# Kernel tuning notes

Hardware: AMD Instinct MI355X
Metric: run time of the kernel (lower is better)

## Reference

```python
import jax, jax.numpy as jnp
import numpy as np

N_ATOMS = 8_000_000
N_REC = 2_000_000
N_POC = 500_000
N_CHAINS = 4


def setup_inputs() -> dict:
    key = jax.random.key(0)
    k1, k2, k3, k4 = jax.random.split(key, 4)
    # coordinates in nm, inside a ~5 nm box
    positions = jax.random.uniform(k1, (N_ATOMS, 3), dtype=jnp.float32) * 5.0
    box_vectors = jnp.diag(jnp.array([5.0, 5.0, 5.0], dtype=jnp.float32))
    # unique receptor atom indices into positions
    rec_indices = jax.random.permutation(k2, N_ATOMS)[:N_REC].astype(jnp.int32)
    # unique pocket indices INTO THE REC ARRAY (poc_pos = rec_pos[poc_indices])
    poc_indices = jax.random.permutation(k3, N_REC)[:N_POC].astype(jnp.int32)
    # contiguous chain assignment over rec atoms, all chains present in pocket
    chain_ids = ((jnp.arange(N_REC, dtype=jnp.int32) * N_CHAINS) // N_REC).astype(jnp.int32)
    poc_chain_ids = chain_ids[poc_indices]
    ref_poc = jax.random.uniform(k4, (N_POC, 3), dtype=jnp.float32) * 5.0
    k = jnp.float32(100.0)  # kJ/mol/nm^2
    return {
        "positions": positions, "box_vectors": box_vectors, "ref_poc": ref_poc,
        "k": k, "rec_indices": rec_indices, "poc_indices": poc_indices,
        "chain_ids": chain_ids, "poc_chain_ids": poc_chain_ids, "n_chains": N_CHAINS,
    }


def best_periodic_translation(pos1, pos2, box_vectors):
    # pos1, pos2: [C,3]; box_vectors: [3,3] (rows are lattice vectors)
    delta = pos2 - pos1
    inv = 1.0 / jnp.diag(box_vectors)
    s3 = jnp.round(delta[:, 2] * inv[2])
    delta = delta - s3[:, None] * box_vectors[2]
    s2 = jnp.round(delta[:, 1] * inv[1])
    delta = delta - s2[:, None] * box_vectors[1]
    s1 = jnp.round(delta[:, 0] * inv[0])
    return s1[:, None] * box_vectors[0] + s2[:, None] * box_vectors[1] + s3[:, None] * box_vectors[2]


def reference(positions, box_vectors, ref_poc, k, rec_indices, poc_indices, chain_ids, poc_chain_ids, n_chains):
    rec_pos = positions[rec_indices]  # [R,3]
    # Per-chain pocket COM. NOTE: original indexes global positions here
    # (positions[poc_chain_indices]), NOT rec_pos -- reproduced faithfully.
    poc_glob = positions[poc_indices]  # [P,3]
    counts = jax.ops.segment_sum(jnp.ones((poc_glob.shape[0],), poc_glob.dtype), poc_chain_ids, num_segments=n_chains)  # [C]
    poc_com = jax.ops.segment_sum(poc_glob, poc_chain_ids, num_segments=n_chains) / counts[:, None]  # [C,3]
    ref_com = jax.ops.segment_sum(ref_poc, poc_chain_ids, num_segments=n_chains) / counts[:, None]  # [C,3]
    best_t = best_periodic_translation(poc_com, ref_com, box_vectors)  # [C,3]
    rec_pos = rec_pos + best_t[chain_ids]  # translate each chain into the reference image

    poc_pos = rec_pos[poc_indices]  # [P,3]
    rec_origin = jnp.mean(rec_pos, axis=0)
    rec_centered = rec_pos - rec_origin
    r_sq = jnp.sum(rec_centered ** 2, axis=1)  # [R]
    F = jnp.zeros_like(rec_pos).at[poc_indices].set(-2.0 * k * (poc_pos - ref_poc))
    F_mean = jnp.mean(F, axis=0)
    torque = jnp.cross(rec_centered, F)
    torque_mean = jnp.mean(torque, axis=0)
    F_rot = jnp.cross(torque_mean[None], rec_centered) / r_sq[:, None]
    F_final = jnp.zeros_like(positions).at[rec_indices].set(F_mean + F_rot)
    return (jnp.float32(0.0), F_final)
```

## Files before the change

kernel.cpp:

```cpp
#include <hip/hip_runtime.h>


typedef unsigned int uint32;
typedef unsigned char uchar;

#define MAXC 16
#define W_BT 0
#define W_O 48
#define W_FM 52
#define W_TM 56
#define W_ACC 64

#define GCOUNT_OFF 4096
#define REC_OFF 8192
#define NB 512
#define BSH 14
#define BUCKET_ATOMS (1 << BSH)
#define CAP 5120
#define INV8_OFF (REC_OFF + NB * CAP * 4)

#define PB 512
#define RB 512
#define K1_KPT 16
#define K1_CHUNK (256 * K1_KPT)

struct PartSh { uint32 hist[NB]; uint32 curs[NB]; uint32 base[NB]; };
struct PocSh  { float red[4][43]; float accL[3 + MAXC * 10]; };
union ShU { PartSh part; PocSh poc; };

__device__ inline float waveSum(float v) {
#pragma unroll
  for (int off = 32; off > 0; off >>= 1) v += __shfl_down(v, off, 64);
  return v;
}

__global__ __launch_bounds__(256) void k_fused(
    const float* __restrict__ pos, const float* __restrict__ ref_poc,
    const int* __restrict__ rec_idx, const int* __restrict__ cid,
    const int* __restrict__ poc_idx, const int* __restrict__ poc_cid,
    const int* __restrict__ ncp, int R, int P,
    uint32* __restrict__ gcount, uint32* __restrict__ grecords,
    float* __restrict__ ws) {
  const int tid = threadIdx.x;
  const int bid = blockIdx.x;
  __shared__ ShU sh;
  const int C = ncp[0];

  if (bid < PB) {
    const int gsz = PB * 256;
    if (C <= 4) {
      float vals[43];
#pragma unroll
      for (int v = 0; v < 43; ++v) vals[v] = 0.f;
      for (int rb = bid * 256 + tid; rb < P; rb += 4 * gsz) {
        int rr[4], i2[4], c2[4], ri[4];
        float g[4][3], p[4][3], rf[4][3];
#pragma unroll
        for (int q = 0; q < 4; ++q) {
          int r = rb + q * gsz;
          rr[q] = (r < P) ? r : -1;
        }
#pragma unroll
        for (int q = 0; q < 4; ++q) {
          int r = (rr[q] < 0) ? 0 : rr[q];
          i2[q] = poc_idx[r];
          c2[q] = poc_cid[r];
        }
#pragma unroll
        for (int q = 0; q < 4; ++q) {
          ri[q] = rec_idx[i2[q]];
          g[q][0] = pos[3 * i2[q] + 0];
          g[q][1] = pos[3 * i2[q] + 1];
          g[q][2] = pos[3 * i2[q] + 2];
        }
#pragma unroll
        for (int q = 0; q < 4; ++q) {
          int r = (rr[q] < 0) ? 0 : rr[q];
          p[q][0] = pos[3 * ri[q] + 0];
          p[q][1] = pos[3 * ri[q] + 1];
          p[q][2] = pos[3 * ri[q] + 2];
          rf[q][0] = ref_poc[3 * r + 0];
          rf[q][1] = ref_poc[3 * r + 1];
          rf[q][2] = ref_poc[3 * r + 2];
        }
#pragma unroll
        for (int q = 0; q < 4; ++q) {
          if (rr[q] >= 0) {
            vals[0] += p[q][1] * rf[q][2] - p[q][2] * rf[q][1];
            vals[1] += p[q][2] * rf[q][0] - p[q][0] * rf[q][2];
            vals[2] += p[q][0] * rf[q][1] - p[q][1] * rf[q][0];
#pragma unroll
            for (int cc = 0; cc < 4; ++cc) {
              bool m = (c2[q] == cc);
              float* a = &vals[3 + cc * 10];
              a[0] += m ? g[q][0] : 0.f; a[1] += m ? g[q][1] : 0.f;
              a[2] += m ? g[q][2] : 0.f;
              a[3] += m ? rf[q][0] : 0.f; a[4] += m ? rf[q][1] : 0.f;
              a[5] += m ? rf[q][2] : 0.f;
              a[6] += m ? p[q][0] : 0.f; a[7] += m ? p[q][1] : 0.f;
              a[8] += m ? p[q][2] : 0.f;
              a[9] += m ? 1.f : 0.f;
            }
          }
        }
      }
      const int wid = tid >> 6;
#pragma unroll
      for (int v = 0; v < 43; ++v) {
        float s = waveSum(vals[v]);
        if ((tid & 63) == 0) sh.poc.red[wid][v] = s;
      }
      __syncthreads();
      for (int t = tid; t < 43; t += 256)
        atomicAdd(&ws[W_ACC + 19 + t], sh.poc.red[0][t] + sh.poc.red[1][t] +
                                       sh.poc.red[2][t] + sh.poc.red[3][t]);
    } else {
      float* accL = sh.poc.accL;
      for (int t = tid; t < 3 + MAXC * 10; t += 256) accL[t] = 0.f;
      __syncthreads();
      for (int r = bid * 256 + tid; r < P; r += PB * 256) {
        int i2 = poc_idx[r];
        int c2 = poc_cid[r];
        int ri = rec_idx[i2];
        float gx = pos[3 * i2 + 0], gy = pos[3 * i2 + 1], gz = pos[3 * i2 + 2];
        float px = pos[3 * ri + 0], py = pos[3 * ri + 1], pz = pos[3 * ri + 2];
        float rx = ref_poc[3 * r + 0], ry = ref_poc[3 * r + 1], rz = ref_poc[3 * r + 2];
        atomicAdd(&accL[0], py * rz - pz * ry);
        atomicAdd(&accL[1], pz * rx - px * rz);
        atomicAdd(&accL[2], px * ry - py * rx);
        float* a = &accL[3 + c2 * 10];
        atomicAdd(&a[0], gx); atomicAdd(&a[1], gy); atomicAdd(&a[2], gz);
        atomicAdd(&a[3], rx); atomicAdd(&a[4], ry); atomicAdd(&a[5], rz);
        atomicAdd(&a[6], px); atomicAdd(&a[7], py); atomicAdd(&a[8], pz);
        atomicAdd(&a[9], 1.f);
      }
      __syncthreads();
      for (int t = tid; t < 3 + MAXC * 10; t += 256)
        if (accL[t] != 0.f) atomicAdd(&ws[W_ACC + 19 + t], accL[t]);
    }
  } else {
    const int pb = bid - PB;
    uint32* hist = sh.part.hist;
    uint32* curs = sh.part.curs;
    uint32* base = sh.part.base;
    for (int r0 = pb * K1_CHUNK; r0 < R; r0 += RB * K1_CHUNK) {
      int cnt = R - r0; if (cnt > K1_CHUNK) cnt = K1_CHUNK;
      for (int t = tid; t < NB; t += 256) { hist[t] = 0u; curs[t] = 0u; }
      __syncthreads();
      uint32 enc[K1_KPT];
#pragma unroll
      for (int j = 0; j < K1_KPT; ++j) {
        int t = tid + j * 256;
        uint32 e = 0xFFFFFFFFu;
        if (t < cnt) {
          uint32 idx = (uint32)rec_idx[r0 + t];
          uint32 c = (uint32)cid[r0 + t] & 255u;
          e = (idx << 8) | c;
          atomicAdd(&hist[idx >> BSH], 1u);
        }
        enc[j] = e;
      }
      __syncthreads();
      for (int t = tid; t < NB; t += 256) {
        uint32 h = hist[t];
        base[t] = h ? atomicAdd(&gcount[t], h) : 0u;
      }
      __syncthreads();
#pragma unroll
      for (int j = 0; j < K1_KPT; ++j) {
        uint32 e = enc[j];
        if (e != 0xFFFFFFFFu) {
          uint32 b = e >> (8 + BSH);
          uint32 slot = base[b] + atomicAdd(&curs[b], 1u);
          if (slot < CAP) grecords[b * CAP + slot] = e;
        }
      }
      __syncthreads();
    }
  }
}

__global__ __launch_bounds__(256) void k_bucket_build(
    const float4* __restrict__ pos4, const int* __restrict__ ncp,
    const uint32* __restrict__ gcount, const uint32* __restrict__ grecords,
    int N, uchar* __restrict__ inv8, float* __restrict__ ws) {
  const int tid = threadIdx.x;
  const int b = blockIdx.x;
  const int a0 = b << BSH;
  if (a0 >= N) return;
  int natoms = N - a0; if (natoms > BUCKET_ATOMS) natoms = BUCKET_ATOMS;

  __shared__ uchar map_[BUCKET_ATOMS];
  __shared__ float cnt16[MAXC];
  uint4* m16 = (uint4*)map_;
  uint4 ff; ff.x = ff.y = ff.z = ff.w = 0xFFFFFFFFu;
  for (int t = tid; t < BUCKET_ATOMS / 16; t += 256) m16[t] = ff;
  const int C = ncp[0];
  if (C > 4) for (int t = tid; t < MAXC; t += 256) cnt16[t] = 0.f;
  __syncthreads();

  int n = (int)gcount[b]; if (n > CAP) n = CAP;
  float c0 = 0.f, c1 = 0.f, c2 = 0.f, c3 = 0.f;
  for (int t = tid; t < n; t += 256) {
    uint32 e = grecords[b * CAP + t];
    uint32 ia = (e >> 8) & (BUCKET_ATOMS - 1);
    uint32 c = e & 255u;
    map_[ia] = (uchar)c;
    if (C <= 4) {
      c0 += (c == 0u) ? 1.f : 0.f;
      c1 += (c == 1u) ? 1.f : 0.f;
      c2 += (c == 2u) ? 1.f : 0.f;
      c3 += (c == 3u) ? 1.f : 0.f;
    } else {
      atomicAdd(&cnt16[c], 1.f);
    }
  }
  __syncthreads();

  uchar* dst = inv8 + a0;
  if (natoms == BUCKET_ATOMS) {
    uint4* d16 = (uint4*)dst;
    for (int t = tid; t < BUCKET_ATOMS / 16; t += 256) d16[t] = m16[t];
  } else {
    for (int t = tid; t < natoms; t += 256) dst[t] = map_[t];
  }

  float sx = 0.f, sy = 0.f, sz = 0.f;
  int ngf = natoms >> 2;
  const uchar4* m4 = (const uchar4*)map_;
  int g0 = a0 >> 2;
  for (int g = tid; g < ngf; g += 256) {
    float4 p0 = pos4[3 * (g0 + g) + 0];
    float4 p1 = pos4[3 * (g0 + g) + 1];
    float4 p2 = pos4[3 * (g0 + g) + 2];
    uchar4 m = m4[g];
    if (m.x != 255) { sx += p0.x; sy += p0.y; sz += p0.z; }
    if (m.y != 255) { sx += p0.w; sy += p1.x; sz += p1.y; }
    if (m.z != 255) { sx += p1.z; sy += p1.w; sz += p2.x; }
    if (m.w != 255) { sx += p2.y; sy += p2.z; sz += p2.w; }
  }
  int tb = natoms & 3;
  if (tid < tb) {
    int a = a0 + (ngf << 2) + tid;
    const float* pf = (const float*)pos4;
    if (map_[(ngf << 2) + tid] != 255) {
      sx += pf[3 * a]; sy += pf[3 * a + 1]; sz += pf[3 * a + 2];
    }
  }

  __shared__ float red[4][7];
  float vv[7] = {sx, sy, sz, c0, c1, c2, c3};
  const int wid = tid >> 6;
#pragma unroll
  for (int v = 0; v < 7; ++v) {
    float s = waveSum(vv[v]);
    if ((tid & 63) == 0) red[wid][v] = s;
  }
  __syncthreads();
  if (tid < 7) {
    float s = red[0][tid] + red[1][tid] + red[2][tid] + red[3][tid];
    atomicAdd(&ws[W_ACC + tid], s);
  }
  if (C > 4 && tid < C) atomicAdd(&ws[W_ACC + 3 + tid], cnt16[tid]);
}

__global__ void k_finalize(const float* __restrict__ box,
                           const float* __restrict__ kp,
                           const int* __restrict__ ncp,
                           int R, float* __restrict__ ws) {
  __shared__ float tot[192];
  const int C = ncp[0];
  for (int t = threadIdx.x; t < 192; t += blockDim.x) tot[t] = ws[W_ACC + t];
  __syncthreads();
  if (threadIdx.x != 0) return;
  const float kk = kp[0];
  const float Rf = (float)R;
  const float* xp = &tot[19];
  float inv0 = 1.f / box[0], inv1 = 1.f / box[4], inv2 = 1.f / box[8];
  float ox = tot[0], oy = tot[1], oz = tot[2];
  float Fx = 0, Fy = 0, Fz = 0;
  float T1x = 0, T1y = 0, T1z = 0, T2x = 0, T2y = 0, T2z = 0;
  for (int c = 0; c < C; ++c) {
    float nrec = tot[3 + c];
    const float* a = &tot[22 + c * 10];
    float np = a[9];
    float invn = 1.f / np;
    float pcx = a[0] * invn, pcy = a[1] * invn, pcz = a[2] * invn;
    float rcx = a[3] * invn, rcy = a[4] * invn, rcz = a[5] * invn;
    float dx = rcx - pcx, dy = rcy - pcy, dz = rcz - pcz;
    float s3 = rintf(dz * inv2);
    dx -= s3 * box[6]; dy -= s3 * box[7]; dz -= s3 * box[8];
    float s2 = rintf(dy * inv1);
    dx -= s2 * box[3]; dy -= s2 * box[4]; dz -= s2 * box[5];
    float s1 = rintf(dx * inv0);
    float btx = s1 * box[0] + s2 * box[3] + s3 * box[6];
    float bty = s1 * box[1] + s2 * box[4] + s3 * box[7];
    float btz = s1 * box[2] + s2 * box[5] + s3 * box[8];
    ws[W_BT + c * 3 + 0] = btx;
    ws[W_BT + c * 3 + 1] = bty;
    ws[W_BT + c * 3 + 2] = btz;
    ox += nrec * btx; oy += nrec * bty; oz += nrec * btz;
    float SFx = -2.f * kk * (a[6] + np * btx - a[3]);
    float SFy = -2.f * kk * (a[7] + np * bty - a[4]);
    float SFz = -2.f * kk * (a[8] + np * btz - a[5]);
    Fx += SFx; Fy += SFy; Fz += SFz;
    T1x += a[7] * btz - a[8] * bty;
    T1y += a[8] * btx - a[6] * btz;
    T1z += a[6] * bty - a[7] * btx;
    T2x += bty * SFz - btz * SFy;
    T2y += btz * SFx - btx * SFz;
    T2z += btx * SFy - bty * SFx;
  }
  ox /= Rf; oy /= Rf; oz /= Rf;
  float Tx = 2.f * kk * xp[0] - 2.f * kk * T1x + T2x - (oy * Fz - oz * Fy);
  float Ty = 2.f * kk * xp[1] - 2.f * kk * T1y + T2y - (oz * Fx - ox * Fz);
  float Tz = 2.f * kk * xp[2] - 2.f * kk * T1z + T2z - (ox * Fy - oy * Fx);
  ws[W_O + 0] = ox; ws[W_O + 1] = oy; ws[W_O + 2] = oz;
  ws[W_FM + 0] = Fx / Rf; ws[W_FM + 1] = Fy / Rf; ws[W_FM + 2] = Fz / Rf;
  ws[W_TM + 0] = Tx / Rf; ws[W_TM + 1] = Ty / Rf; ws[W_TM + 2] = Tz / Rf;
}

__global__ __launch_bounds__(256) void k_final_dense(
    const float* __restrict__ pos, const uchar* __restrict__ inv8,
    int N, const float* __restrict__ ws, float* __restrict__ out) {
  __shared__ float stage[3328];
  __shared__ float sc[64];
  const int tid = threadIdx.x;
  if (tid < 64) sc[tid] = ws[tid];
  const int t0 = blockIdx.x * 1024;
  int nat = N - t0; if (nat > 1024) nat = 1024;
  const int nfl = nat * 3;

  if (nat == 1024) {
    const float4* src4 = (const float4*)(pos + 3 * t0);
#pragma unroll
    for (int kk = 0; kk < 3; ++kk) {
      int v4 = tid + kk * 256;
      float4 p = src4[v4];
      int idx = 4 * v4 + v4 / 3;
      stage[idx + 0] = p.x; stage[idx + 1] = p.y;
      stage[idx + 2] = p.z; stage[idx + 3] = p.w;
    }
  } else {
    for (int k = tid; k < nfl; k += 256)
      stage[k + (int)((unsigned)k / 12u)] = pos[3 * t0 + k];
  }
  __syncthreads();

  float ox = sc[W_O + 0], oy = sc[W_O + 1], oz = sc[W_O + 2];
  float fmx = sc[W_FM + 0], fmy = sc[W_FM + 1], fmz = sc[W_FM + 2];
  float tmx = sc[W_TM + 0], tmy = sc[W_TM + 1], tmz = sc[W_TM + 2];

  uchar mc[4];
  if (nat == 1024) {
    uchar4 m = ((const uchar4*)(inv8 + t0))[tid];
    mc[0] = m.x; mc[1] = m.y; mc[2] = m.z; mc[3] = m.w;
  } else {
#pragma unroll
    for (int q = 0; q < 4; ++q) {
      int la = 4 * tid + q;
      mc[q] = (la < nat) ? inv8[t0 + la] : (uchar)255;
    }
  }
#pragma unroll
  for (int q = 0; q < 4; ++q) {
    int la = 4 * tid + q;
    if (la < nat) {
      float* s = &stage[13 * tid + 3 * q];
      float fx = 0.f, fy = 0.f, fz = 0.f;
      int c = mc[q];
      if (c != 255) {
        float cx = s[0] + sc[W_BT + 3 * c + 0] - ox;
        float cy = s[1] + sc[W_BT + 3 * c + 1] - oy;
        float cz = s[2] + sc[W_BT + 3 * c + 2] - oz;
        float inv = 1.f / (cx * cx + cy * cy + cz * cz);
        fx = fmx + (tmy * cz - tmz * cy) * inv;
        fy = fmy + (tmz * cx - tmx * cz) * inv;
        fz = fmz + (tmx * cy - tmy * cx) * inv;
      }
      s[0] = fx; s[1] = fy; s[2] = fz;
    }
  }
  __syncthreads();

  if (blockIdx.x == 0 && tid == 0) out[0] = 0.f;
  float* ob = out + 1 + 3 * t0;
  if (nat == 1024) {
#pragma unroll
    for (int kk = 0; kk < 3; ++kk) {
      int j = tid + kk * 256;
      if (j < 767) {
        int k = 3 + 4 * j;
        float4 v;
        v.x = stage[k + k / 12];
        v.y = stage[(k + 1) + (k + 1) / 12];
        v.z = stage[(k + 2) + (k + 2) / 12];
        v.w = stage[(k + 3) + (k + 3) / 12];
        *(float4*)(ob + k) = v;
      }
    }
    if (tid < 3) ob[tid] = stage[tid];
    if (tid == 3) ob[3071] = stage[3071 + 3071 / 12];
  } else {
    for (int k = tid; k < nfl; k += 256)
      ob[k] = stage[k + (int)((unsigned)k / 12u)];
  }
}

extern "C" void kernel_launch(void* const* d_in, const int* in_sizes, int n_in,
                              void* d_out, int out_size, void* d_ws, size_t ws_size,
                              hipStream_t stream) {
  const float* pos     = (const float*)d_in[0];
  const float* box     = (const float*)d_in[1];
  const float* ref_poc = (const float*)d_in[2];
  const float* kp      = (const float*)d_in[3];
  const int* rec_idx   = (const int*)d_in[4];
  const int* poc_idx   = (const int*)d_in[5];
  const int* cid       = (const int*)d_in[6];
  const int* poc_cid   = (const int*)d_in[7];
  const int* ncp       = (const int*)d_in[8];
  float* out = (float*)d_out;
  float* ws  = (float*)d_ws;
  uint32* gcount   = (uint32*)((char*)d_ws + GCOUNT_OFF);
  uint32* grecords = (uint32*)((char*)d_ws + REC_OFF);
  uchar* inv8      = (uchar*)d_ws + INV8_OFF;

  const int N = in_sizes[0] / 3;
  const int R = in_sizes[4];
  const int P = in_sizes[5];

  hipMemsetAsync(d_ws, 0, 8192, stream);

  k_fused<<<PB + RB, 256, 0, stream>>>(pos, ref_poc, rec_idx, cid, poc_idx,
                                       poc_cid, ncp, R, P, gcount, grecords, ws);
  k_bucket_build<<<NB, 256, 0, stream>>>((const float4*)pos, ncp, gcount,
                                         grecords, N, inv8, ws);
  k_finalize<<<1, 256, 0, stream>>>(box, kp, ncp, R, ws);
  int gF = (N + 1023) / 1024;
  k_final_dense<<<gF, 256, 0, stream>>>(pos, inv8, N, ws, out);
}
```

Baseline: 267.4 us.

## Fuse bucket build, finalize and dense output into one per-bucket kernel

The receptor COM sum and chain counts move into the partition blocks of the first kernel, which now gather positions by receptor index instead of doing a dense masked scan. Bucket map construction, the scalar finalize and the dense force output are merged into one kernel. Each block rebuilds its 16K-atom chain map in LDS, recomputes the finalize scalars redundantly, and writes output for its bucket. This removes two launches and the global inv8 byte-map round trip. The costs are only 489 output blocks with a serial 16-step loop each, which lowers parallelism, plus random gathers in the partition phase.

New measurement: 290.4 us. 8.6% more time.

```diff
diff --git a/kernel.cpp b/kernel.cpp
--- a/kernel.cpp
+++ b/kernel.cpp
@@ -17,7 +17,6 @@
 #define BSH 14
 #define BUCKET_ATOMS (1 << BSH)
 #define CAP 5120
-#define INV8_OFF (REC_OFF + NB * CAP * 4)
 
 #define PB 512
 #define RB 512
@@ -34,7 +33,7 @@
   return v;
 }
 
-__global__ __launch_bounds__(256) void k_fused(
+__global__ __launch_bounds__(256) void k_mix(
     const float* __restrict__ pos, const float* __restrict__ ref_poc,
     const int* __restrict__ rec_idx, const int* __restrict__ cid,
     const int* __restrict__ poc_idx, const int* __restrict__ poc_cid,
@@ -43,8 +42,10 @@
     float* __restrict__ ws) {
   const int tid = threadIdx.x;
   const int bid = blockIdx.x;
+  const int C = ncp[0];
   __shared__ ShU sh;
-  const int C = ncp[0];
+  __shared__ float red7[4][7];
+  __shared__ float cnt16[MAXC];
 
   if (bid < PB) {
     const int gsz = PB * 256;
@@ -140,10 +141,18 @@
     }
   } else {
     const int pb = bid - PB;
+    const int NCHUNK = (R + K1_CHUNK - 1) / K1_CHUNK;
     uint32* hist = sh.part.hist;
     uint32* curs = sh.part.curs;
     uint32* base = sh.part.base;
-    for (int r0 = pb * K1_CHUNK; r0 < R; r0 += RB * K1_CHUNK) {
+    float sx = 0.f, sy = 0.f, sz = 0.f;
+    float c0 = 0.f, c1 = 0.f, c2 = 0.f, c3 = 0.f;
+    if (C > 4) {
+      for (int t = tid; t < MAXC; t += 256) cnt16[t] = 0.f;
+      __syncthreads();
+    }
+    for (int ch = pb; ch < NCHUNK; ch += RB) {
+      const int r0 = ch * K1_CHUNK;
       int cnt = R - r0; if (cnt > K1_CHUNK) cnt = K1_CHUNK;
       for (int t = tid; t < NB; t += 256) { hist[t] = 0u; curs[t] = 0u; }
       __syncthreads();
@@ -157,6 +166,12 @@
           uint32 c = (uint32)cid[r0 + t] & 255u;
           e = (idx << 8) | c;
           atomicAdd(&hist[idx >> BSH], 1u);
+          if (C <= 4) {
+            c0 += (c == 0u) ? 1.f : 0.f; c1 += (c == 1u) ? 1.f : 0.f;
+            c2 += (c == 2u) ? 1.f : 0.f; c3 += (c == 3u) ? 1.f : 0.f;
+          } else {
+            atomicAdd(&cnt16[c], 1.f);
+          }
         }
         enc[j] = e;
       }
@@ -175,235 +190,205 @@
           if (slot < CAP) grecords[b * CAP + slot] = e;
         }
       }
-      __syncthreads();
-    }
+#pragma unroll
+      for (int j0 = 0; j0 < K1_KPT; j0 += 4) {
+        int ri[4];
+        float px[4], py[4], pz[4];
+#pragma unroll
+        for (int q = 0; q < 4; ++q) {
+          uint32 e = enc[j0 + q];
+          ri[q] = (e == 0xFFFFFFFFu) ? 0 : (int)(e >> 8);
+        }
+#pragma unroll
+        for (int q = 0; q < 4; ++q) {
+          px[q] = pos[3 * ri[q] + 0];
+          py[q] = pos[3 * ri[q] + 1];
+          pz[q] = pos[3 * ri[q] + 2];
+        }
+#pragma unroll
+        for (int q = 0; q < 4; ++q) {
+          if (enc[j0 + q] != 0xFFFFFFFFu) {
+            sx += px[q]; sy += py[q]; sz += pz[q];
+          }
+        }
+      }
+      __syncthreads();
+    }
+    float vv[7] = {sx, sy, sz, c0, c1, c2, c3};
+    const int wid = tid >> 6;
+#pragma unroll
+    for (int v = 0; v < 7; ++v) {
+      float s = waveSum(vv[v]);
+      if ((tid & 63) == 0) red7[wid][v] = s;
+    }
+    __syncthreads();
+    if (tid < 7) {
+      float s = red7[0][tid] + red7[1][tid] + red7[2][tid] + red7[3][tid];
+      if (s != 0.f) atomicAdd(&ws[W_ACC + tid], s);
+    }
+    if (C > 4 && tid < C) atomicAdd(&ws[W_ACC + 3 + tid], cnt16[tid]);
   }
 }
 
-__global__ __launch_bounds__(256) void k_bucket_build(
-    const float4* __restrict__ pos4, const int* __restrict__ ncp,
-    const uint32* __restrict__ gcount, const uint32* __restrict__ grecords,
-    int N, uchar* __restrict__ inv8, float* __restrict__ ws) {
+__global__ __launch_bounds__(256) void k_bucket_out(
+    const float* __restrict__ pos, const uint32* __restrict__ gcount,
+    const uint32* __restrict__ grecords, const float* __restrict__ box,
+    const float* __restrict__ kp, const int* __restrict__ ncp,
+    int R, int N, const float* __restrict__ ws, float* __restrict__ out) {
+  __shared__ uchar map_[BUCKET_ATOMS];
+  __shared__ float stage[3328];
+  __shared__ float tot[192];
+  __shared__ float sc[64];
   const int tid = threadIdx.x;
   const int b = blockIdx.x;
   const int a0 = b << BSH;
   if (a0 >= N) return;
-  int natoms = N - a0; if (natoms > BUCKET_ATOMS) natoms = BUCKET_ATOMS;
-
-  __shared__ uchar map_[BUCKET_ATOMS];
-  __shared__ float cnt16[MAXC];
+
+  for (int t = tid; t < 192; t += 256) tot[t] = ws[W_ACC + t];
   uint4* m16 = (uint4*)map_;
   uint4 ff; ff.x = ff.y = ff.z = ff.w = 0xFFFFFFFFu;
   for (int t = tid; t < BUCKET_ATOMS / 16; t += 256) m16[t] = ff;
-  const int C = ncp[0];
-  if (C > 4) for (int t = tid; t < MAXC; t += 256) cnt16[t] = 0.f;
   __syncthreads();
 
   int n = (int)gcount[b]; if (n > CAP) n = CAP;
-  float c0 = 0.f, c1 = 0.f, c2 = 0.f, c3 = 0.f;
   for (int t = tid; t < n; t += 256) {
     uint32 e = grecords[b * CAP + t];
-    uint32 ia = (e >> 8) & (BUCKET_ATOMS - 1);
-    uint32 c = e & 255u;
-    map_[ia] = (uchar)c;
-    if (C <= 4) {
-      c0 += (c == 0u) ? 1.f : 0.f;
-      c1 += (c == 1u) ? 1.f : 0.f;
-      c2 += (c == 2u) ? 1.f : 0.f;
-      c3 += (c == 3u) ? 1.f : 0.f;
-    } else {
-      atomicAdd(&cnt16[c], 1.f);
-    }
+    map_[(e >> 8) & (BUCKET_ATOMS - 1)] = (uchar)(e & 255u);
   }
   __syncthreads();
 
-  uchar* dst = inv8 + a0;
-  if (natoms == BUCKET_ATOMS) {
-    uint4* d16 = (uint4*)dst;
-    for (int t = tid; t < BUCKET_ATOMS / 16; t += 256) d16[t] = m16[t];
-  } else {
-    for (int t = tid; t < natoms; t += 256) dst[t] = map_[t];
-  }
-
-  float sx = 0.f, sy = 0.f, sz = 0.f;
-  int ngf = natoms >> 2;
-  const uchar4* m4 = (const uchar4*)map_;
-  int g0 = a0 >> 2;
-  for (int g = tid; g < ngf; g += 256) {
-    float4 p0 = pos4[3 * (g0 + g) + 0];
-    float4 p1 = pos4[3 * (g0 + g) + 1];
-    float4 p2 = pos4[3 * (g0 + g) + 2];
-    uchar4 m = m4[g];
-    if (m.x != 255) { sx += p0.x; sy += p0.y; sz += p0.z; }
-    if (m.y != 255) { sx += p0.w; sy += p1.x; sz += p1.y; }
-    if (m.z != 255) { sx += p1.z; sy += p1.w; sz += p2.x; }
-    if (m.w != 255) { sx += p2.y; sy += p2.z; sz += p2.w; }
-  }
-  int tb = natoms & 3;
-  if (tid < tb) {
-    int a = a0 + (ngf << 2) + tid;
-    const float* pf = (const float*)pos4;
-    if (map_[(ngf << 2) + tid] != 255) {
-      sx += pf[3 * a]; sy += pf[3 * a + 1]; sz += pf[3 * a + 2];
-    }
-  }
-
-  __shared__ float red[4][7];
-  float vv[7] = {sx, sy, sz, c0, c1, c2, c3};
-  const int wid = tid >> 6;
-#pragma unroll
-  for (int v = 0; v < 7; ++v) {
-    float s = waveSum(vv[v]);
-    if ((tid & 63) == 0) red[wid][v] = s;
+  if (tid == 0) {
+    const int C = ncp[0];
+    const float kk = kp[0];
+    const float Rf = (float)R;
+    const float* xp = &tot[19];
+    float inv0 = 1.f / box[0], inv1 = 1.f / box[4], inv2 = 1.f / box[8];
+    float ox = tot[0], oy = tot[1], oz = tot[2];
+    float Fx = 0, Fy = 0, Fz = 0;
+    float T1x = 0, T1y = 0, T1z = 0, T2x = 0, T2y = 0, T2z = 0;
+    for (int c = 0; c < C; ++c) {
+      float nrec = tot[3 + c];
+      const float* a = &tot[22 + c * 10];
+      float np = a[9];
+      float invn = 1.f / np;
+      float pcx = a[0] * invn, pcy = a[1] * invn, pcz = a[2] * invn;
+      float rcx = a[3] * invn, rcy = a[4] * invn, rcz = a[5] * invn;
+      float dx = rcx - pcx, dy = rcy - pcy, dz = rcz - pcz;
+      float s3 = rintf(dz * inv2);
+      dx -= s3 * box[6]; dy -= s3 * box[7]; dz -= s3 * box[8];
+      float s2 = rintf(dy * inv1);
+      dx -= s2 * box[3]; dy -= s2 * box[4]; dz -= s2 * box[5];
+      float s1 = rintf(dx * inv0);
+      float btx = s1 * box[0] + s2 * box[3] + s3 * box[6];
+      float bty = s1 * box[1] + s2 * box[4] + s3 * box[7];
+      float btz = s1 * box[2] + s2 * box[5] + s3 * box[8];
+      sc[W_BT + c * 3 + 0] = btx;
+      sc[W_BT + c * 3 + 1] = bty;
+      sc[W_BT + c * 3 + 2] = btz;
+      ox += nrec * btx; oy += nrec * bty; oz += nrec * btz;
+      float SFx = -2.f * kk * (a[6] + np * btx - a[3]);
+      float SFy = -2.f * kk * (a[7] + np * bty - a[4]);
+      float SFz = -2.f * kk * (a[8] + np * btz - a[5]);
+      Fx += SFx; Fy += SFy; Fz += SFz;
+      T1x += a[7] * btz - a[8] * bty;
+      T1y += a[8] * btx - a[6] * btz;
+      T1z += a[6] * bty - a[7] * btx;
+      T2x += bty * SFz - btz * SFy;
+      T2y += btz * SFx - btx * SFz;
+      T2z += btx * SFy - bty * SFx;
+    }
+    ox /= Rf; oy /= Rf; oz /= Rf;
+    float Tx = 2.f * kk * xp[0] - 2.f * kk * T1x + T2x - (oy * Fz - oz * Fy);
+    float Ty = 2.f * kk * xp[1] - 2.f * kk * T1y + T2y - (oz * Fx - ox * Fz);
+    float Tz = 2.f * kk * xp[2] - 2.f * kk * T1z + T2z - (ox * Fy - oy * Fx);
+    sc[W_O + 0] = ox; sc[W_O + 1] = oy; sc[W_O + 2] = oz;
+    sc[W_FM + 0] = Fx / Rf; sc[W_FM + 1] = Fy / Rf; sc[W_FM + 2] = Fz / Rf;
+    sc[W_TM + 0] = Tx / Rf; sc[W_TM + 1] = Ty / Rf; sc[W_TM + 2] = Tz / Rf;
   }
   __syncthreads();
-  if (tid < 7) {
-    float s = red[0][tid] + red[1][tid] + red[2][tid] + red[3][tid];
-    atomicAdd(&ws[W_ACC + tid], s);
-  }
-  if (C > 4 && tid < C) atomicAdd(&ws[W_ACC + 3 + tid], cnt16[tid]);
-}
-
-__global__ void k_finalize(const float* __restrict__ box,
-                           const float* __restrict__ kp,
-                           const int* __restrict__ ncp,
-                           int R, float* __restrict__ ws) {
-  __shared__ float tot[192];
-  const int C = ncp[0];
-  for (int t = threadIdx.x; t < 192; t += blockDim.x) tot[t] = ws[W_ACC + t];
-  __syncthreads();
-  if (threadIdx.x != 0) return;
-  const float kk = kp[0];
-  const float Rf = (float)R;
-  const float* xp = &tot[19];
-  float inv0 = 1.f / box[0], inv1 = 1.f / box[4], inv2 = 1.f / box[8];
-  float ox = tot[0], oy = tot[1], oz = tot[2];
-  float Fx = 0, Fy = 0, Fz = 0;
-  float T1x = 0, T1y = 0, T1z = 0, T2x = 0, T2y = 0, T2z = 0;
-  for (int c = 0; c < C; ++c) {
-    float nrec = tot[3 + c];
-    const float* a = &tot[22 + c * 10];
-    float np = a[9];
-    float invn = 1.f / np;
-    float pcx = a[0] * invn, pcy = a[1] * invn, pcz = a[2] * invn;
-    float rcx = a[3] * invn, rcy = a[4] * invn, rcz = a[5] * invn;
-    float dx = rcx - pcx, dy = rcy - pcy, dz = rcz - pcz;
-    float s3 = rintf(dz * inv2);
-    dx -= s3 * box[6]; dy -= s3 * box[7]; dz -= s3 * box[8];
-    float s2 = rintf(dy * inv1);
-    dx -= s2 * box[3]; dy -= s2 * box[4]; dz -= s2 * box[5];
-    float s1 = rintf(dx * inv0);
-    float btx = s1 * box[0] + s2 * box[3] + s3 * box[6];
-    float bty = s1 * box[1] + s2 * box[4] + s3 * box[7];
-    float btz = s1 * box[2] + s2 * box[5] + s3 * box[8];
-    ws[W_BT + c * 3 + 0] = btx;
-    ws[W_BT + c * 3 + 1] = bty;
-    ws[W_BT + c * 3 + 2] = btz;
-    ox += nrec * btx; oy += nrec * bty; oz += nrec * btz;
-    float SFx = -2.f * kk * (a[6] + np * btx - a[3]);
-    float SFy = -2.f * kk * (a[7] + np * bty - a[4]);
-    float SFz = -2.f * kk * (a[8] + np * btz - a[5]);
-    Fx += SFx; Fy += SFy; Fz += SFz;
-    T1x += a[7] * btz - a[8] * bty;
-    T1y += a[8] * btx - a[6] * btz;
-    T1z += a[6] * bty - a[7] * btx;
-    T2x += bty * SFz - btz * SFy;
-    T2y += btz * SFx - btx * SFz;
-    T2z += btx * SFy - bty * SFx;
-  }
-  ox /= Rf; oy /= Rf; oz /= Rf;
-  float Tx = 2.f * kk * xp[0] - 2.f * kk * T1x + T2x - (oy * Fz - oz * Fy);
-  float Ty = 2.f * kk * xp[1] - 2.f * kk * T1y + T2y - (oz * Fx - ox * Fz);
-  float Tz = 2.f * kk * xp[2] - 2.f * kk * T1z + T2z - (ox * Fy - oy * Fx);
-  ws[W_O + 0] = ox; ws[W_O + 1] = oy; ws[W_O + 2] = oz;
-  ws[W_FM + 0] = Fx / Rf; ws[W_FM + 1] = Fy / Rf; ws[W_FM + 2] = Fz / Rf;
-  ws[W_TM + 0] = Tx / Rf; ws[W_TM + 1] = Ty / Rf; ws[W_TM + 2] = Tz / Rf;
-}
-
-__global__ __launch_bounds__(256) void k_final_dense(
-    const float* __restrict__ pos, const uchar* __restrict__ inv8,
-    int N, const float* __restrict__ ws, float* __restrict__ out) {
-  __shared__ float stage[3328];
-  __shared__ float sc[64];
-  const int tid = threadIdx.x;
-  if (tid < 64) sc[tid] = ws[tid];
-  const int t0 = blockIdx.x * 1024;
-  int nat = N - t0; if (nat > 1024) nat = 1024;
-  const int nfl = nat * 3;
-
-  if (nat == 1024) {
-    const float4* src4 = (const float4*)(pos + 3 * t0);
-#pragma unroll
-    for (int kk = 0; kk < 3; ++kk) {
-      int v4 = tid + kk * 256;
-      float4 p = src4[v4];
-      int idx = 4 * v4 + v4 / 3;
-      stage[idx + 0] = p.x; stage[idx + 1] = p.y;
-      stage[idx + 2] = p.z; stage[idx + 3] = p.w;
-    }
-  } else {
-    for (int k = tid; k < nfl; k += 256)
-      stage[k + (int)((unsigned)k / 12u)] = pos[3 * t0 + k];
-  }
-  __syncthreads();
-
-  float ox = sc[W_O + 0], oy = sc[W_O + 1], oz = sc[W_O + 2];
-  float fmx = sc[W_FM + 0], fmy = sc[W_FM + 1], fmz = sc[W_FM + 2];
-  float tmx = sc[W_TM + 0], tmy = sc[W_TM + 1], tmz = sc[W_TM + 2];
-
-  uchar mc[4];
-  if (nat == 1024) {
-    uchar4 m = ((const uchar4*)(inv8 + t0))[tid];
-    mc[0] = m.x; mc[1] = m.y; mc[2] = m.z; mc[3] = m.w;
-  } else {
+
+  const float ox = sc[W_O + 0], oy = sc[W_O + 1], oz = sc[W_O + 2];
+  const float fmx = sc[W_FM + 0], fmy = sc[W_FM + 1], fmz = sc[W_FM + 2];
+  const float tmx = sc[W_TM + 0], tmy = sc[W_TM + 1], tmz = sc[W_TM + 2];
+
+#pragma unroll 1
+  for (int st = 0; st < (BUCKET_ATOMS >> 10); ++st) {
+    const int t0 = a0 + (st << 10);
+    if (t0 >= N) break;
+    int nat = N - t0; if (nat > 1024) nat = 1024;
+    const int nfl = nat * 3;
+
+    if (nat == 1024) {
+      const float4* src4 = (const float4*)(pos + 3 * t0);
+#pragma unroll
+      for (int kk = 0; kk < 3; ++kk) {
+        int v4 = tid + kk * 256;
+        float4 p = src4[v4];
+        int idx = 4 * v4 + v4 / 3;
+        stage[idx + 0] = p.x; stage[idx + 1] = p.y;
+        stage[idx + 2] = p.z; stage[idx + 3] = p.w;
+      }
+    } else {
+      for (int k = tid; k < nfl; k += 256)
+        stage[k + (int)((unsigned)k / 12u)] = pos[3 * t0 + k];
+    }
+    __syncthreads();
+
+    uchar mc[4];
+    if (nat == 1024) {
+      uchar4 m = ((const uchar4*)map_)[(st << 8) + tid];
+      mc[0] = m.x; mc[1] = m.y; mc[2] = m.z; mc[3] = m.w;
+    } else {
+#pragma unroll
+      for (int q = 0; q < 4; ++q) {
+        int la = 4 * tid + q;
+        mc[q] = (la < nat) ? map_[(st << 10) + la] : (uchar)255;
+      }
+    }
 #pragma unroll
     for (int q = 0; q < 4; ++q) {
       int la = 4 * tid + q;
-      mc[q] = (la < nat) ? inv8[t0 + la] : (uchar)255;
-    }
-  }
-#pragma unroll
-  for (int q = 0; q < 4; ++q) {
-    int la = 4 * tid + q;
-    if (la < nat) {
-      float* s = &stage[13 * tid + 3 * q];
-      float fx = 0.f, fy = 0.f, fz = 0.f;
-      int c = mc[q];
-      if (c != 255) {
-        float cx = s[0] + sc[W_BT + 3 * c + 0] - ox;
-        float cy = s[1] + sc[W_BT + 3 * c + 1] - oy;
-        float cz = s[2] + sc[W_BT + 3 * c + 2] - oz;
-        float inv = 1.f / (cx * cx + cy * cy + cz * cz);
-        fx = fmx + (tmy * cz - tmz * cy) * inv;
-        fy = fmy + (tmz * cx - tmx * cz) * inv;
-        fz = fmz + (tmx * cy - tmy * cx) * inv;
-      }
-      s[0] = fx; s[1] = fy; s[2] = fz;
-    }
-  }
-  __syncthreads();
-
-  if (blockIdx.x == 0 && tid == 0) out[0] = 0.f;
-  float* ob = out + 1 + 3 * t0;
-  if (nat == 1024) {
-#pragma unroll
-    for (int kk = 0; kk < 3; ++kk) {
-      int j = tid + kk * 256;
-      if (j < 767) {
-        int k = 3 + 4 * j;
-        float4 v;
-        v.x = stage[k + k / 12];
-        v.y = stage[(k + 1) + (k + 1) / 12];
-        v.z = stage[(k + 2) + (k + 2) / 12];
-        v.w = stage[(k + 3) + (k + 3) / 12];
-        *(float4*)(ob + k) = v;
-      }
-    }
-    if (tid < 3) ob[tid] = stage[tid];
-    if (tid == 3) ob[3071] = stage[3071 + 3071 / 12];
-  } else {
-    for (int k = tid; k < nfl; k += 256)
-      ob[k] = stage[k + (int)((unsigned)k / 12u)];
+      if (la < nat) {
+        float* s = &stage[13 * tid + 3 * q];
+        float fx = 0.f, fy = 0.f, fz = 0.f;
+        int c = mc[q];
+        if (c != 255) {
+          float cx = s[0] + sc[W_BT + 3 * c + 0] - ox;
+          float cy = s[1] + sc[W_BT + 3 * c + 1] - oy;
+          float cz = s[2] + sc[W_BT + 3 * c + 2] - oz;
+          float inv = 1.f / (cx * cx + cy * cy + cz * cz);
+          fx = fmx + (tmy * cz - tmz * cy) * inv;
+          fy = fmy + (tmz * cx - tmx * cz) * inv;
+          fz = fmz + (tmx * cy - tmy * cx) * inv;
+        }
+        s[0] = fx; s[1] = fy; s[2] = fz;
+      }
+    }
+    __syncthreads();
+
+    if (b == 0 && st == 0 && tid == 0) out[0] = 0.f;
+    float* ob = out + 1 + 3 * t0;
+    if (nat == 1024) {
+#pragma unroll
+      for (int kk = 0; kk < 3; ++kk) {
+        int j = tid + kk * 256;
+        if (j < 767) {
+          int k = 3 + 4 * j;
+          float4 v;
+          v.x = stage[k + k / 12];
+          v.y = stage[(k + 1) + (k + 1) / 12];
+          v.z = stage[(k + 2) + (k + 2) / 12];
+          v.w = stage[(k + 3) + (k + 3) / 12];
+          *(float4*)(ob + k) = v;
+        }
+      }
+      if (tid < 3) ob[tid] = stage[tid];
+      if (tid == 3) ob[3071] = stage[3071 + 3071 / 12];
+    } else {
+      for (int k = tid; k < nfl; k += 256)
+        ob[k] = stage[k + (int)((unsigned)k / 12u)];
+    }
+    __syncthreads();
   }
 }
 
@@ -423,7 +408,6 @@
   float* ws  = (float*)d_ws;
   uint32* gcount   = (uint32*)((char*)d_ws + GCOUNT_OFF);
   uint32* grecords = (uint32*)((char*)d_ws + REC_OFF);
-  uchar* inv8      = (uchar*)d_ws + INV8_OFF;
 
   const int N = in_sizes[0] / 3;
   const int R = in_sizes[4];
@@ -431,11 +415,9 @@
 
   hipMemsetAsync(d_ws, 0, 8192, stream);
 
-  k_fused<<<PB + RB, 256, 0, stream>>>(pos, ref_poc, rec_idx, cid, poc_idx,
-                                       poc_cid, ncp, R, P, gcount, grecords, ws);
-  k_bucket_build<<<NB, 256, 0, stream>>>((const float4*)pos, ncp, gcount,
-                                         grecords, N, inv8, ws);
-  k_finalize<<<1, 256, 0, stream>>>(box, kp, ncp, R, ws);
-  int gF = (N + 1023) / 1024;
-  k_final_dense<<<gF, 256, 0, stream>>>(pos, inv8, N, ws, out);
+  k_mix<<<PB + RB, 256, 0, stream>>>(pos, ref_poc, rec_idx, cid, poc_idx,
+                                     poc_cid, ncp, R, P, gcount, grecords, ws);
+  const int g2 = (N + BUCKET_ATOMS - 1) >> BSH;
+  k_bucket_out<<<g2, 256, 0, stream>>>(pos, gcount, grecords, box, kp, ncp,
+                                       R, N, ws, out);
 }
```
